# Optimization experiments

Measured on AMD Instinct MI355X. Metric: run time of the kernel, lower is better.

## Reference

```python
import jax, jax.numpy as jnp
import numpy as np

N = 131072   # utterances
D = 256      # embedding dim
C = 1024     # speakers (unique labels)


def setup_inputs() -> dict:
    key = jax.random.key(0)
    k1, k2 = jax.random.split(key)
    embeddings = jax.random.normal(k1, (N, D), dtype=jnp.float32)
    labels = jax.random.randint(k2, (N,), 0, C, dtype=jnp.int32)
    w = jnp.asarray(10.0, dtype=jnp.float32)
    b = jnp.asarray(-5.0, dtype=jnp.float32)
    return {"embeddings": embeddings, "labels": labels, "w": w, "b": b}


def reference(embeddings, labels, w, b):
    # Segment mean -> centroids [C, D]. With N >> C all labels occur, so
    # torch.unique(labels) == arange(C) and target == labels.
    sums = jax.ops.segment_sum(embeddings, labels, num_segments=C)
    counts = jax.ops.segment_sum(jnp.ones((embeddings.shape[0],), embeddings.dtype),
                                 labels, num_segments=C)
    centroids = sums / counts[:, None]
    # logits [N, C]
    logits = w * jnp.einsum('nd,cd->nc', embeddings, centroids) + b
    logp = jax.nn.log_softmax(logits, axis=-1)
    nll = -jnp.take_along_axis(logp, labels[:, None].astype(jnp.int32), axis=1)[:, 0]
    return jnp.mean(nll)
```

## Files before the change

kernel.cpp:

```cpp
#include <hip/hip_runtime.h>
#include <hip/hip_bf16.h>

#define NROWS 131072
#define DDIM  256
#define CDIM  1024

#define L2E 1.4426950408889634f
#define LN2 0.6931471805599453f

typedef short bf16x8 __attribute__((ext_vector_type(8)));
typedef float f32x4 __attribute__((ext_vector_type(4)));

#define GLOAD_LDS16(g, l) __builtin_amdgcn_global_load_lds( \
    (const __attribute__((address_space(1))) void*)(g),      \
    (__attribute__((address_space(3))) void*)(l), 16, 0, 0)

__device__ __forceinline__ unsigned short f2b(float x) {
    unsigned int u = __builtin_bit_cast(unsigned int, x);
    u = (u + 0x7FFFu + ((u >> 16) & 1u)) >> 16;
    return (unsigned short)u;
}

__global__ void k_prep(const int* __restrict__ labels, int* __restrict__ offsets,
                       int* __restrict__ rowidx, float* __restrict__ out) {
    __shared__ int h[CDIM];
    __shared__ int c[CDIM];
    const int t = threadIdx.x;
    h[t] = 0;
    __syncthreads();
    const int4* l4 = (const int4*)labels;
    for (int i = t; i < NROWS / 4; i += 1024) {
        const int4 v = l4[i];
        atomicAdd(&h[v.x], 1); atomicAdd(&h[v.y], 1);
        atomicAdd(&h[v.z], 1); atomicAdd(&h[v.w], 1);
    }
    __syncthreads();
    const int v = h[t];
    c[t] = v;
    __syncthreads();
    for (int d = 1; d < CDIM; d <<= 1) {
        const int add = (t >= d) ? c[t - d] : 0;
        __syncthreads();
        c[t] += add;
        __syncthreads();
    }
    const int excl = c[t] - v;
    offsets[t] = excl;
    if (t == CDIM - 1) offsets[CDIM] = c[t];
    c[t] = excl;
    if (t == 0) out[0] = 0.0f;
    __syncthreads();
    for (int i = t; i < NROWS / 4; i += 1024) {
        const int4 v4 = l4[i];
        const int base = i * 4;
        int p;
        p = atomicAdd(&c[v4.x], 1); rowidx[p] = base;
        p = atomicAdd(&c[v4.y], 1); rowidx[p] = base + 1;
        p = atomicAdd(&c[v4.z], 1); rowidx[p] = base + 2;
        p = atomicAdd(&c[v4.w], 1); rowidx[p] = base + 3;
    }
}

__global__ void k_centroid(const float* __restrict__ emb, const int* __restrict__ rowidx,
                           const int* __restrict__ offsets, unsigned short* __restrict__ centG) {
    __shared__ f32x4 red[4][64];
    const int cgrp = blockIdx.x;
    const int t = threadIdx.x;
    const int w = t >> 6;
    const int lane = t & 63;
    const int beg = offsets[cgrp], end = offsets[cgrp + 1];

    f32x4 acc = {0.0f, 0.0f, 0.0f, 0.0f};
    for (int i = beg + w * 2; i < end; i += 8) {
        const int row0 = rowidx[i];
        const int row1 = (i + 1 < end) ? rowidx[i + 1] : -1;
        const float4 v0 = *reinterpret_cast<const float4*>(emb + (size_t)row0 * DDIM + lane * 4);
        if (row1 >= 0) {
            const float4 v1 = *reinterpret_cast<const float4*>(emb + (size_t)row1 * DDIM + lane * 4);
            acc[0] += v1.x; acc[1] += v1.y; acc[2] += v1.z; acc[3] += v1.w;
        }
        acc[0] += v0.x; acc[1] += v0.y; acc[2] += v0.z; acc[3] += v0.w;
    }
    red[w][lane] = acc;
    __syncthreads();
    if (t < 32) {
        const float inv = 1.0f / (float)(end - beg);
        f32x4 a = red[0][2 * t], b4 = red[0][2 * t + 1];
#pragma unroll
        for (int ww = 1; ww < 4; ++ww) {
            const f32x4 x = red[ww][2 * t], y = red[ww][2 * t + 1];
            a[0] += x[0]; a[1] += x[1]; a[2] += x[2]; a[3] += x[3];
            b4[0] += y[0]; b4[1] += y[1]; b4[2] += y[2]; b4[3] += y[3];
        }
        uint4 u;
        u.x = (unsigned)f2b(a[0] * inv) | ((unsigned)f2b(a[1] * inv) << 16);
        u.y = (unsigned)f2b(a[2] * inv) | ((unsigned)f2b(a[3] * inv) << 16);
        u.z = (unsigned)f2b(b4[0] * inv) | ((unsigned)f2b(b4[1] * inv) << 16);
        u.w = (unsigned)f2b(b4[2] * inv) | ((unsigned)f2b(b4[3] * inv) << 16);
        const int cc = cgrp >> 6, ctq = (cgrp >> 4) & 3, lr2 = cgrp & 15;
        const int kk = t >> 2, lg2 = t & 3;
        *reinterpret_cast<uint4*>(centG + (size_t)cc * 16384 + ctq * 4096 + kk * 512
                                  + (lg2 * 16 + lr2) * 8) = u;
    }
}

__launch_bounds__(256, 2)
__global__ void k_logits(const float* __restrict__ emb, const int* __restrict__ labels,
                         const unsigned short* __restrict__ centG, const float* __restrict__ wp,
                         float* __restrict__ out) {
    __shared__ unsigned short lds[2][16384];
    char* const Ab = reinterpret_cast<char*>(&lds[0][0]);

    const float wscale = wp[0];
    const int t = threadIdx.x;
    const int w = t >> 6;
    const int lane = t & 63;
    const int lg = lane >> 4;
    const int lr = lane & 15;
    const int rowbase = blockIdx.x * 64;

#pragma unroll
    for (int j = 0; j < 8; ++j) {
        const int J = w * 8 + j;
        GLOAD_LDS16(centG + J * 512 + lane * 8, &lds[1][J * 512]);
    }

    for (int i = 0; i < 16; ++i) {
        const int flat = i * 1024 + t * 4;
        const int row = flat >> 8;
        const int k = flat & 255;
        const float4 v = *reinterpret_cast<const float4*>(emb + (size_t)(rowbase + row) * DDIM + k);
        ushort4 hh;
        hh.x = f2b(v.x); hh.y = f2b(v.y); hh.z = f2b(v.z); hh.w = f2b(v.w);
        const int byte = ((row << 9) + (k << 1)) ^ ((row & 7) << 4);
        *reinterpret_cast<ushort4*>(Ab + byte) = hh;
    }
    __syncthreads();

    bf16x8 af[8];
    {
        const int row = w * 16 + lr;
#pragma unroll
        for (int kk = 0; kk < 8; ++kk) {
            const int byte = ((row << 9) + kk * 64 + lg * 16) ^ ((row & 7) << 4);
            af[kk] = *reinterpret_cast<const bf16x8*>(Ab + byte);
        }
    }
    __syncthreads();

    float m[4], s[4], lv[4];
    int labs[4];
#pragma unroll
    for (int r = 0; r < 4; ++r) {
        m[r] = -1e30f; s[r] = 0.0f; lv[r] = 0.0f;
        labs[r] = labels[rowbase + w * 16 + lg * 4 + r];
    }

    for (int cc = 0; cc < 16; ++cc) {
        if (cc < 15) {
            const unsigned short* src = centG + (cc + 1) * 16384;
#pragma unroll
            for (int j = 0; j < 8; ++j) {
                const int J = w * 8 + j;
                GLOAD_LDS16(src + J * 512 + lane * 8, &lds[cc & 1][J * 512]);
            }
        }
        const unsigned short* bb = &lds[(cc + 1) & 1][lane * 8];
        float vals[4][4];
#pragma unroll
        for (int ct = 0; ct < 4; ++ct) {
            f32x4 acc = {0.0f, 0.0f, 0.0f, 0.0f};
#pragma unroll
            for (int kk = 0; kk < 8; ++kk) {
                const bf16x8 bf = *reinterpret_cast<const bf16x8*>(bb + ct * 4096 + kk * 512);
                acc = __builtin_amdgcn_mfma_f32_16x16x32_bf16(af[kk], bf, acc, 0, 0, 0);
            }
            const int colg = cc * 64 + ct * 16 + lr;
#pragma unroll
            for (int r = 0; r < 4; ++r) {
                const float v = wscale * acc[r];
                vals[ct][r] = v;
                if (colg == labs[r]) lv[r] = v;
            }
        }
#pragma unroll
        for (int r = 0; r < 4; ++r) {
            const float cmax = fmaxf(fmaxf(vals[0][r], vals[1][r]),
                                     fmaxf(vals[2][r], vals[3][r]));
            const float mo = m[r];
            const float mn = fmaxf(mo, cmax);
            const float ssum = exp2f((vals[0][r] - mn) * L2E) + exp2f((vals[1][r] - mn) * L2E)
                             + exp2f((vals[2][r] - mn) * L2E) + exp2f((vals[3][r] - mn) * L2E);
            s[r] = s[r] * exp2f((mo - mn) * L2E) + ssum;
            m[r] = mn;
        }
        __syncthreads();
    }

    float part = 0.0f;
#pragma unroll
    for (int r = 0; r < 4; ++r) {
        float mm = m[r], ss = s[r], ll = lv[r];
#pragma unroll
        for (int off = 1; off < 16; off <<= 1) {
            const float mo = __shfl_xor(mm, off, 64);
            const float so = __shfl_xor(ss, off, 64);
            const float lo = __shfl_xor(ll, off, 64);
            const float mn = fmaxf(mm, mo);
            ss = ss * exp2f((mm - mn) * L2E) + so * exp2f((mo - mn) * L2E);
            mm = mn;
            ll += lo;
        }
        if (lr == 0) {
            const float lse = mm + log2f(ss) * LN2;
            part += (lse - ll);
        }
    }
    if (lr == 0) atomicAdd(out, part * (1.0f / NROWS));
}

extern "C" void kernel_launch(void* const* d_in, const int* in_sizes, int n_in,
                              void* d_out, int out_size, void* d_ws, size_t ws_size,
                              hipStream_t stream) {
    const float* emb = (const float*)d_in[0];
    const int* labels = (const int*)d_in[1];
    const float* wp = (const float*)d_in[2];
    float* out = (float*)d_out;

    int* offsets = (int*)d_ws;
    int* rowidx = (int*)((char*)d_ws + 8192);
    unsigned short* centG = (unsigned short*)((char*)d_ws + 532480);

    k_prep<<<1, 1024, 0, stream>>>(labels, offsets, rowidx, out);
    k_centroid<<<CDIM, 256, 0, stream>>>(emb, rowidx, offsets, centG);
    k_logits<<<NROWS / 64, 256, 0, stream>>>(emb, labels, centG, wp, out);
}
```

Baseline: 456.5 us.

## Parallelize label bucketing and restructure centroid and logits kernels

New measurement: 423.3 us. 7.3% less time.

```diff
diff --git a/kernel.cpp b/kernel.cpp
--- a/kernel.cpp
+++ b/kernel.cpp
@@ -21,48 +21,40 @@
     return (unsigned short)u;
 }
 
-__global__ void k_prep(const int* __restrict__ labels, int* __restrict__ offsets,
-                       int* __restrict__ rowidx, float* __restrict__ out) {
-    __shared__ int h[CDIM];
-    __shared__ int c[CDIM];
+__global__ void k_hist(const int* __restrict__ labels, int* __restrict__ hist) {
+    const int i = blockIdx.x * 256 + threadIdx.x;
+    atomicAdd(&hist[labels[i]], 1);
+}
+
+__global__ void k_scan(const int* __restrict__ hist, int* __restrict__ offsets,
+                       float* __restrict__ out) {
+    __shared__ int tmp[CDIM];
     const int t = threadIdx.x;
-    h[t] = 0;
-    __syncthreads();
-    const int4* l4 = (const int4*)labels;
-    for (int i = t; i < NROWS / 4; i += 1024) {
-        const int4 v = l4[i];
-        atomicAdd(&h[v.x], 1); atomicAdd(&h[v.y], 1);
-        atomicAdd(&h[v.z], 1); atomicAdd(&h[v.w], 1);
-    }
-    __syncthreads();
-    const int v = h[t];
-    c[t] = v;
+    const int v = hist[t];
+    tmp[t] = v;
     __syncthreads();
     for (int d = 1; d < CDIM; d <<= 1) {
-        const int add = (t >= d) ? c[t - d] : 0;
-        __syncthreads();
-        c[t] += add;
-        __syncthreads();
-    }
-    const int excl = c[t] - v;
-    offsets[t] = excl;
-    if (t == CDIM - 1) offsets[CDIM] = c[t];
-    c[t] = excl;
+        const int add = (t >= d) ? tmp[t - d] : 0;
+        __syncthreads();
+        tmp[t] += add;
+        __syncthreads();
+    }
+    offsets[t] = tmp[t] - v;
+    if (t == CDIM - 1) offsets[CDIM] = tmp[t];
     if (t == 0) out[0] = 0.0f;
-    __syncthreads();
-    for (int i = t; i < NROWS / 4; i += 1024) {
-        const int4 v4 = l4[i];
-        const int base = i * 4;
-        int p;
-        p = atomicAdd(&c[v4.x], 1); rowidx[p] = base;
-        p = atomicAdd(&c[v4.y], 1); rowidx[p] = base + 1;
-        p = atomicAdd(&c[v4.z], 1); rowidx[p] = base + 2;
-        p = atomicAdd(&c[v4.w], 1); rowidx[p] = base + 3;
-    }
+}
+
+__global__ void k_scatter(const int* __restrict__ labels, const int* __restrict__ offsets,
+                          int* __restrict__ cursor, int* __restrict__ rowidx) {
+    const int i = blockIdx.x * 256 + threadIdx.x;
+    const int lab = labels[i];
+    const int pos = atomicAdd(&cursor[lab], 1);
+    rowidx[offsets[lab] + pos] = i;
 }
 
 __global__ void k_centroid(const float* __restrict__ emb, const int* __restrict__ rowidx,
                            const int* __restrict__ offsets, unsigned short* __restrict__ centG) {
+    __shared__ int ridx[256];
     __shared__ f32x4 red[4][64];
     const int cgrp = blockIdx.x;
     const int t = threadIdx.x;
@@ -71,15 +63,28 @@
     const int beg = offsets[cgrp], end = offsets[cgrp + 1];
 
     f32x4 acc = {0.0f, 0.0f, 0.0f, 0.0f};
-    for (int i = beg + w * 2; i < end; i += 8) {
-        const int row0 = rowidx[i];
-        const int row1 = (i + 1 < end) ? rowidx[i + 1] : -1;
-        const float4 v0 = *reinterpret_cast<const float4*>(emb + (size_t)row0 * DDIM + lane * 4);
-        if (row1 >= 0) {
-            const float4 v1 = *reinterpret_cast<const float4*>(emb + (size_t)row1 * DDIM + lane * 4);
-            acc[0] += v1.x; acc[1] += v1.y; acc[2] += v1.z; acc[3] += v1.w;
-        }
-        acc[0] += v0.x; acc[1] += v0.y; acc[2] += v0.z; acc[3] += v0.w;
+    for (int base = beg; base < end; base += 256) {
+        const int cnt = min(256, end - base);
+        __syncthreads();
+        if (t < cnt) ridx[t] = rowidx[base + t];
+        __syncthreads();
+        for (int i = w * 4; i < cnt; i += 16) {
+            float4 v[4];
+            int nr = min(4, cnt - i);
+#pragma unroll
+            for (int j = 0; j < 4; ++j) {
+                if (j < nr) {
+                    const int row = ridx[i + j];
+                    v[j] = *reinterpret_cast<const float4*>(emb + (size_t)row * DDIM + lane * 4);
+                } else {
+                    v[j] = make_float4(0.f, 0.f, 0.f, 0.f);
+                }
+            }
+#pragma unroll
+            for (int j = 0; j < 4; ++j) {
+                acc[0] += v[j].x; acc[1] += v[j].y; acc[2] += v[j].z; acc[3] += v[j].w;
+            }
+        }
     }
     red[w][lane] = acc;
     __syncthreads();
@@ -104,49 +109,41 @@
     }
 }
 
-__launch_bounds__(256, 2)
+__launch_bounds__(512, 4)
 __global__ void k_logits(const float* __restrict__ emb, const int* __restrict__ labels,
                          const unsigned short* __restrict__ centG, const float* __restrict__ wp,
                          float* __restrict__ out) {
     __shared__ unsigned short lds[2][16384];
-    char* const Ab = reinterpret_cast<char*>(&lds[0][0]);
-
-    const float wscale = wp[0];
+
+    const float wl2e = wp[0] * L2E;
     const int t = threadIdx.x;
     const int w = t >> 6;
     const int lane = t & 63;
     const int lg = lane >> 4;
     const int lr = lane & 15;
-    const int rowbase = blockIdx.x * 64;
-
-#pragma unroll
-    for (int j = 0; j < 8; ++j) {
-        const int J = w * 8 + j;
+    const int rowbase = blockIdx.x * 128;
+    const int myrow = rowbase + w * 16 + lr;
+
+#pragma unroll
+    for (int j = 0; j < 4; ++j) {
+        const int J = w * 4 + j;
         GLOAD_LDS16(centG + J * 512 + lane * 8, &lds[1][J * 512]);
     }
-
-    for (int i = 0; i < 16; ++i) {
-        const int flat = i * 1024 + t * 4;
-        const int row = flat >> 8;
-        const int k = flat & 255;
-        const float4 v = *reinterpret_cast<const float4*>(emb + (size_t)(rowbase + row) * DDIM + k);
-        ushort4 hh;
-        hh.x = f2b(v.x); hh.y = f2b(v.y); hh.z = f2b(v.z); hh.w = f2b(v.w);
-        const int byte = ((row << 9) + (k << 1)) ^ ((row & 7) << 4);
-        *reinterpret_cast<ushort4*>(Ab + byte) = hh;
-    }
-    __syncthreads();
+    __builtin_amdgcn_sched_barrier(0);
 
     bf16x8 af[8];
-    {
-        const int row = w * 16 + lr;
-#pragma unroll
-        for (int kk = 0; kk < 8; ++kk) {
-            const int byte = ((row << 9) + kk * 64 + lg * 16) ^ ((row & 7) << 4);
-            af[kk] = *reinterpret_cast<const bf16x8*>(Ab + byte);
-        }
-    }
-    __syncthreads();
+#pragma unroll
+    for (int kk = 0; kk < 8; ++kk) {
+        const float* src = emb + (size_t)myrow * DDIM + kk * 32 + lg * 8;
+        const float4 a0 = *reinterpret_cast<const float4*>(src);
+        const float4 a1 = *reinterpret_cast<const float4*>(src + 4);
+        bf16x8 f;
+        f[0] = (short)f2b(a0.x); f[1] = (short)f2b(a0.y);
+        f[2] = (short)f2b(a0.z); f[3] = (short)f2b(a0.w);
+        f[4] = (short)f2b(a1.x); f[5] = (short)f2b(a1.y);
+        f[6] = (short)f2b(a1.z); f[7] = (short)f2b(a1.w);
+        af[kk] = f;
+    }
 
     float m[4], s[4], lv[4];
     int labs[4];
@@ -156,14 +153,18 @@
         labs[r] = labels[rowbase + w * 16 + lg * 4 + r];
     }
 
+    asm volatile("s_waitcnt vmcnt(0)" ::: "memory");
+    __builtin_amdgcn_s_barrier();
+
     for (int cc = 0; cc < 16; ++cc) {
         if (cc < 15) {
             const unsigned short* src = centG + (cc + 1) * 16384;
 #pragma unroll
-            for (int j = 0; j < 8; ++j) {
-                const int J = w * 8 + j;
+            for (int j = 0; j < 4; ++j) {
+                const int J = w * 4 + j;
                 GLOAD_LDS16(src + J * 512 + lane * 8, &lds[cc & 1][J * 512]);
             }
+            __builtin_amdgcn_sched_barrier(0);
         }
         const unsigned short* bb = &lds[(cc + 1) & 1][lane * 8];
         float vals[4][4];
@@ -178,23 +179,24 @@
             const int colg = cc * 64 + ct * 16 + lr;
 #pragma unroll
             for (int r = 0; r < 4; ++r) {
-                const float v = wscale * acc[r];
-                vals[ct][r] = v;
-                if (colg == labs[r]) lv[r] = v;
+                const float e = wl2e * acc[r];
+                vals[ct][r] = e;
+                if (colg == labs[r]) lv[r] = e;
             }
         }
 #pragma unroll
         for (int r = 0; r < 4; ++r) {
-            const float cmax = fmaxf(fmaxf(vals[0][r], vals[1][r]),
-                                     fmaxf(vals[2][r], vals[3][r]));
+            const float cmax = fmaxf(fmaxf(fmaxf(vals[0][r], vals[1][r]), vals[2][r]),
+                                     vals[3][r]);
             const float mo = m[r];
             const float mn = fmaxf(mo, cmax);
-            const float ssum = exp2f((vals[0][r] - mn) * L2E) + exp2f((vals[1][r] - mn) * L2E)
-                             + exp2f((vals[2][r] - mn) * L2E) + exp2f((vals[3][r] - mn) * L2E);
-            s[r] = s[r] * exp2f((mo - mn) * L2E) + ssum;
+            const float ssum = exp2f(vals[0][r] - mn) + exp2f(vals[1][r] - mn)
+                             + exp2f(vals[2][r] - mn) + exp2f(vals[3][r] - mn);
+            s[r] = s[r] * exp2f(mo - mn) + ssum;
             m[r] = mn;
         }
-        __syncthreads();
+        asm volatile("s_waitcnt vmcnt(0)" ::: "memory");
+        __builtin_amdgcn_s_barrier();
     }
 
     float part = 0.0f;
@@ -207,16 +209,13 @@
             const float so = __shfl_xor(ss, off, 64);
             const float lo = __shfl_xor(ll, off, 64);
             const float mn = fmaxf(mm, mo);
-            ss = ss * exp2f((mm - mn) * L2E) + so * exp2f((mo - mn) * L2E);
+            ss = ss * exp2f(mm - mn) + so * exp2f(mo - mn);
             mm = mn;
             ll += lo;
         }
-        if (lr == 0) {
-            const float lse = mm + log2f(ss) * LN2;
-            part += (lse - ll);
-        }
-    }
-    if (lr == 0) atomicAdd(out, part * (1.0f / NROWS));
+        if (lr == 0) part += (mm + log2f(ss) - ll);
+    }
+    if (lr == 0) atomicAdd(out, part * (LN2 / NROWS));
 }
 
 extern "C" void kernel_launch(void* const* d_in, const int* in_sizes, int n_in,
@@ -227,11 +226,17 @@
     const float* wp = (const float*)d_in[2];
     float* out = (float*)d_out;
 
-    int* offsets = (int*)d_ws;
-    int* rowidx = (int*)((char*)d_ws + 8192);
-    unsigned short* centG = (unsigned short*)((char*)d_ws + 532480);
-
-    k_prep<<<1, 1024, 0, stream>>>(labels, offsets, rowidx, out);
+    int* hist = (int*)d_ws;
+    int* cursor = (int*)((char*)d_ws + 4096);
+    int* offsets = (int*)((char*)d_ws + 8192);
+    int* rowidx = (int*)((char*)d_ws + 16384);
+    unsigned short* centG = (unsigned short*)((char*)d_ws + 540672);
+
+    hipMemsetAsync(d_ws, 0, 8192, stream);
+
+    k_hist<<<NROWS / 256, 256, 0, stream>>>(labels, hist);
+    k_scan<<<1, CDIM, 0, stream>>>(hist, offsets, out);
+    k_scatter<<<NROWS / 256, 256, 0, stream>>>(labels, offsets, cursor, rowidx);
     k_centroid<<<CDIM, 256, 0, stream>>>(emb, rowidx, offsets, centG);
-    k_logits<<<NROWS / 64, 256, 0, stream>>>(emb, labels, centG, wp, out);
-}
+    k_logits<<<NROWS / 128, 512, 0, stream>>>(emb, labels, centG, wp, out);
+}
```
